# Kernel optimization log

Hardware: AMD Instinct MI355X
Metric: run time of the kernel (lower is better)

Reference implementation:

```python
import jax, jax.numpy as jnp
import numpy as np

N_NODES = 50000
N_EDGES = 800000
D_IN = 64
D_OUT = 64


def setup_inputs() -> dict:
    key = jax.random.key(0)
    k1, k2, k3, k4, k5 = jax.random.split(key, 5)
    x = jax.random.normal(k1, (N_NODES, D_IN), dtype=jnp.float32)
    senders = jax.random.randint(k2, (N_EDGES,), 0, N_NODES, dtype=jnp.int32)
    receivers = jax.random.randint(k3, (N_EDGES,), 0, N_NODES, dtype=jnp.int32)
    # eqx.nn.Linear params: weight [out, in], bias [out]
    weight = jax.random.normal(k4, (D_OUT, D_IN), dtype=jnp.float32) / np.sqrt(D_IN)
    bias = jax.random.normal(k5, (D_OUT,), dtype=jnp.float32) * 0.01
    return {"x": x, "senders": senders, "receivers": receivers, "weight": weight, "bias": bias}


def reference(x, senders, receivers, weight, bias):
    n = x.shape[0]
    # jraph.GraphConvolution applies update_node_fn (the Linear) FIRST
    h = x @ weight.T + bias  # [N, D_OUT]
    # add self edges
    self_idx = jnp.arange(n, dtype=senders.dtype)
    cs = jnp.concatenate([senders, self_idx])
    cr = jnp.concatenate([receivers, self_idx])
    ones = jnp.ones(cs.shape, dtype=h.dtype)
    sender_deg = jax.ops.segment_sum(ones, cs, num_segments=n)
    receiver_deg = jax.ops.segment_sum(ones, cr, num_segments=n)
    # symmetric normalization: D^{-1/2} A D^{-1/2}
    h = h * jax.lax.rsqrt(jnp.maximum(sender_deg, 1.0))[:, None]
    h = jax.ops.segment_sum(h[cs], cr, num_segments=n)  # gather -> scatter-add
    h = h * jax.lax.rsqrt(jnp.maximum(receiver_deg, 1.0))[:, None]
    return jax.nn.leaky_relu(h)  # default negative_slope=0.01
```

## Files before the change

### kernel.cpp

```cpp
#include <hip/hip_runtime.h>

#define N_NODES 50000
#define N_EDGES 800000
#define D 64
#define NB 196
#define BSZ 256
#define NSLICE 256
#define SLICE_E 3136
#define SLICE_I4 784
#define E4 (N_EDGES / 4)

__device__ __forceinline__ ushort f2bf(float f) {
    unsigned u = __float_as_uint(f);
    unsigned r = u + 0x7fffu + ((u >> 16) & 1u);
    return (ushort)(r >> 16);
}
__device__ __forceinline__ void acc8(const uint4 a, float* acc) {
    acc[0] += __uint_as_float(a.x << 16);
    acc[1] += __uint_as_float(a.x & 0xffff0000u);
    acc[2] += __uint_as_float(a.y << 16);
    acc[3] += __uint_as_float(a.y & 0xffff0000u);
    acc[4] += __uint_as_float(a.z << 16);
    acc[5] += __uint_as_float(a.z & 0xffff0000u);
    acc[6] += __uint_as_float(a.w << 16);
    acc[7] += __uint_as_float(a.w & 0xffff0000u);
}

__global__ __launch_bounds__(1024) void part1_kernel(
        const int* __restrict__ s, const int* __restrict__ r,
        unsigned* __restrict__ prc, unsigned char* __restrict__ psc,
        int* __restrict__ rcnt, int* __restrict__ scnt,
        int* __restrict__ roffg, int* __restrict__ soffg) {
    __shared__ unsigned lprc[SLICE_E];
    __shared__ unsigned char lpsc[SLICE_E];
    __shared__ int rcur[NB], scur[NB];
    __shared__ int rof[NB], sof[NB];
    const int tid = threadIdx.x, sl = blockIdx.x;
    for (int i = tid; i < NB; i += 1024) { rcur[i] = 0; scur[i] = 0; }
    __syncthreads();

    int e4 = sl * SLICE_I4 + tid;
    const bool act = (tid < SLICE_I4) && (e4 < E4);
    int4 rv, sv;
    if (act) {
        rv = ((const int4*)r)[e4];
        sv = ((const int4*)s)[e4];
        atomicAdd(&rcur[rv.x >> 8], 1); atomicAdd(&rcur[rv.y >> 8], 1);
        atomicAdd(&rcur[rv.z >> 8], 1); atomicAdd(&rcur[rv.w >> 8], 1);
        atomicAdd(&scur[sv.x >> 8], 1); atomicAdd(&scur[sv.y >> 8], 1);
        atomicAdd(&scur[sv.z >> 8], 1); atomicAdd(&scur[sv.w >> 8], 1);
    }
    __syncthreads();

    {
        const int wv = tid >> 6, lane = tid & 63;
        if (wv < 2) {
            const int* cnt = wv ? scur : rcur;
            int* off = wv ? sof : rof;
            const int base = lane * 4;
            int c0 = (base + 0 < NB) ? cnt[base + 0] : 0;
            int c1 = (base + 1 < NB) ? cnt[base + 1] : 0;
            int c2 = (base + 2 < NB) ? cnt[base + 2] : 0;
            int c3 = (base + 3 < NB) ? cnt[base + 3] : 0;
            int sum = c0 + c1 + c2 + c3;
            int sv_ = sum;
            #pragma unroll
            for (int o = 1; o < 64; o <<= 1) {
                int u = __shfl_up(sv_, o);
                if (lane >= o) sv_ += u;
            }
            int excl = sv_ - sum;
            if (base + 0 < NB) off[base + 0] = excl;
            if (base + 1 < NB) off[base + 1] = excl + c0;
            if (base + 2 < NB) off[base + 2] = excl + c0 + c1;
            if (base + 3 < NB) off[base + 3] = excl + c0 + c1 + c2;
        }
    }
    __syncthreads();

    if (tid < NB) {
        rcnt[sl * NB + tid] = rcur[tid];
        scnt[sl * NB + tid] = scur[tid];
        roffg[sl * NB + tid] = rof[tid];
        soffg[sl * NB + tid] = sof[tid];
    }
    __syncthreads();

    if (act) {
        int ri[4] = {rv.x, rv.y, rv.z, rv.w};
        int si[4] = {sv.x, sv.y, sv.z, sv.w};
        #pragma unroll
        for (int k = 0; k < 4; ++k) {
            int pos = atomicAdd(&rof[ri[k] >> 8], 1);
            lprc[pos] = ((unsigned)(ri[k] & 255) << 16) | (unsigned)si[k];
            int pos2 = atomicAdd(&sof[si[k] >> 8], 1);
            lpsc[pos2] = (unsigned char)(si[k] & 255);
        }
    }
    __syncthreads();

    if (tid < SLICE_I4)
        ((uint4*)(prc + (size_t)sl * SLICE_E))[tid] = ((const uint4*)lprc)[tid];
    if (tid < SLICE_E / 16)
        ((uint4*)(psc + (size_t)sl * SLICE_E))[tid] = ((const uint4*)lpsc)[tid];
}

__global__ __launch_bounds__(256, 4) void post_kernel(
        const unsigned* __restrict__ prc, const unsigned char* __restrict__ psc,
        const int* __restrict__ rcnt, const int* __restrict__ scnt,
        const int* __restrict__ roffg, const int* __restrict__ soffg,
        int* __restrict__ rowoff, ushort* __restrict__ csr16,
        const float* __restrict__ x, const float* __restrict__ w,
        const float* __restrict__ bias, ushort* __restrict__ h16) {
    __shared__ int sc[256];
    __shared__ int h4[BSZ];
    __shared__ float wlds[64 * 68];
    __shared__ float xlds[64 * 68];
    __shared__ float slds[BSZ];
    __shared__ float blds[64];
    const int tid = threadIdx.x;

    if (blockIdx.x >= NB) {
        const int b = blockIdx.x - NB;
        h4[tid] = 0;
        if (tid < 64) blds[tid] = bias[tid];
        __syncthreads();
        {
            int sl = tid;
            int c = scnt[sl * NB + b];
            const unsigned char* cell = psc + (size_t)sl * SLICE_E + soffg[sl * NB + b];
            for (int i = 0; i < c; ++i) atomicAdd(&h4[cell[i]], 1);
        }
        __syncthreads();
        slds[tid] = rsqrtf((float)(h4[tid] + 1));
        #pragma unroll
        for (int q = 0; q < 4; ++q) {
            int idx = q * 256 + tid;
            int o = idx >> 4, k4 = idx & 15;
            float4 wv = ((const float4*)w)[idx];
            *(float4*)&wlds[o * 68 + k4 * 4] = wv;
        }
        __syncthreads();

        const int t15 = tid & 15;
        const int g = tid >> 4;
        for (int tile = 0; tile < 4; ++tile) {
            const int nb = b * BSZ + tile * 64;
            #pragma unroll
            for (int q = 0; q < 4; ++q) {
                int idx = q * 256 + tid;
                int nl = idx >> 4, k4 = idx & 15;
                int n = nb + nl;
                float4 xv = (n < N_NODES) ? ((const float4*)x)[n * 16 + k4]
                                          : make_float4(0.f, 0.f, 0.f, 0.f);
                *(float4*)&xlds[nl * 68 + k4 * 4] = xv;
            }
            __syncthreads();

            float acc[4][4];
            #pragma unroll
            for (int i = 0; i < 4; ++i)
                #pragma unroll
                for (int j = 0; j < 4; ++j) acc[i][j] = 0.f;

            #pragma unroll 2
            for (int k4 = 0; k4 < 16; ++k4) {
                float4 wv0 = *(const float4*)&wlds[(t15     ) * 68 + k4 * 4];
                float4 wv1 = *(const float4*)&wlds[(t15 + 16) * 68 + k4 * 4];
                float4 wv2 = *(const float4*)&wlds[(t15 + 32) * 68 + k4 * 4];
                float4 wv3 = *(const float4*)&wlds[(t15 + 48) * 68 + k4 * 4];
                #pragma unroll
                for (int i = 0; i < 4; ++i) {
                    float4 xv = *(const float4*)&xlds[(g * 4 + i) * 68 + k4 * 4];
                    acc[i][0] += xv.x * wv0.x + xv.y * wv0.y + xv.z * wv0.z + xv.w * wv0.w;
                    acc[i][1] += xv.x * wv1.x + xv.y * wv1.y + xv.z * wv1.z + xv.w * wv1.w;
                    acc[i][2] += xv.x * wv2.x + xv.y * wv2.y + xv.z * wv2.z + xv.w * wv2.w;
                    acc[i][3] += xv.x * wv3.x + xv.y * wv3.y + xv.z * wv3.z + xv.w * wv3.w;
                }
            }

            #pragma unroll
            for (int i = 0; i < 4; ++i) {
                int nl = g * 4 + i;
                int n = nb + nl;
                if (n < N_NODES) {
                    float scl = slds[tile * 64 + nl];
                    h16[n * D + t15     ] = f2bf((acc[i][0] + blds[t15     ]) * scl);
                    h16[n * D + t15 + 16] = f2bf((acc[i][1] + blds[t15 + 16]) * scl);
                    h16[n * D + t15 + 32] = f2bf((acc[i][2] + blds[t15 + 32]) * scl);
                    h16[n * D + t15 + 48] = f2bf((acc[i][3] + blds[t15 + 48]) * scl);
                }
            }
            __syncthreads();
        }
        return;
    }

    const int b = blockIdx.x;
    int tot = 0;
    if (tid < NB) {
        for (int sl = 0; sl < NSLICE; ++sl) tot += rcnt[sl * NB + tid];
    }
    sc[tid] = tot;
    __syncthreads();
    for (int o = 1; o < 256; o <<= 1) {
        int u = (tid >= o) ? sc[tid - o] : 0;
        __syncthreads();
        sc[tid] += u;
        __syncthreads();
    }
    const int rb = (b == 0) ? 0 : sc[b - 1];
    __syncthreads();

    h4[tid] = 0;
    __syncthreads();
    {
        int sl = tid;
        int c = rcnt[sl * NB + b];
        const unsigned* cell = prc + (size_t)sl * SLICE_E + roffg[sl * NB + b];
        for (int i = 0; i < c; ++i) atomicAdd(&h4[cell[i] >> 16], 1);
    }
    __syncthreads();

    int v = h4[tid];
    sc[tid] = v;
    __syncthreads();
    for (int o = 1; o < 256; o <<= 1) {
        int u = (tid >= o) ? sc[tid - o] : 0;
        __syncthreads();
        sc[tid] += u;
        __syncthreads();
    }
    int excl = sc[tid] - v;
    int n = b * BSZ + tid;
    if (n < N_NODES) rowoff[n] = rb + excl;
    h4[tid] = rb + excl;
    if (b == NB - 1 && tid == 0) rowoff[N_NODES] = N_EDGES;
    __syncthreads();

    {
        int sl = tid;
        int c = rcnt[sl * NB + b];
        const unsigned* cell = prc + (size_t)sl * SLICE_E + roffg[sl * NB + b];
        for (int i = 0; i < c; ++i) {
            unsigned pw = cell[i];
            int pos = atomicAdd(&h4[pw >> 16], 1);
            csr16[pos] = (ushort)(pw & 0xffffu);
        }
    }
}

__global__ __launch_bounds__(256) void gather_kernel(
        const ushort* __restrict__ h16, const int* __restrict__ rowoff,
        const ushort* __restrict__ csr16, float* __restrict__ out) {
    const int lane = threadIdx.x & 63;
    const int q = lane & 7;
    const int g = lane >> 3;
    const int n = blockIdx.x * 4 + (threadIdx.x >> 6);
    if (n >= N_NODES) return;

    float acc[8];
    #pragma unroll
    for (int k = 0; k < 8; ++k) acc[k] = 0.f;

    const int base = rowoff[n];
    const int cnt = rowoff[n + 1] - base;

    for (int j0 = 0; j0 < cnt; j0 += 64) {
        int m = cnt - j0; if (m > 64) m = 64;
        int my = (lane < m) ? (int)csr16[base + j0 + lane] : 0;
        int t = 0;
        for (; t + 16 <= m; t += 16) {
            int s0 = __shfl(my, t + g);
            int s1 = __shfl(my, t + 8 + g);
            uint4 a = *(const uint4*)&h16[s0 * D + q * 8];
            uint4 b = *(const uint4*)&h16[s1 * D + q * 8];
            acc8(a, acc);
            acc8(b, acc);
        }
        for (; t < m; t += 8) {
            int e = t + g;
            int ee = (e < m) ? e : 0;
            int s0 = __shfl(my, ee);
            if (e < m) {
                uint4 a = *(const uint4*)&h16[s0 * D + q * 8];
                acc8(a, acc);
            }
        }
    }

    #pragma unroll
    for (int k = 0; k < 8; ++k) acc[k] += __shfl_xor(acc[k], 8);
    #pragma unroll
    for (int k = 0; k < 8; ++k) acc[k] += __shfl_xor(acc[k], 16);
    #pragma unroll
    for (int k = 0; k < 8; ++k) acc[k] += __shfl_xor(acc[k], 32);

    uint4 sv = *(const uint4*)&h16[n * D + q * 8];
    acc8(sv, acc);
    float sc = rsqrtf((float)(cnt + 1));
    float o[8];
    #pragma unroll
    for (int k = 0; k < 8; ++k) {
        float vv = acc[k] * sc;
        o[k] = vv > 0.f ? vv : 0.01f * vv;
    }
    if (g == 0) {
        *(float4*)(out + n * D + q * 8)     = make_float4(o[0], o[1], o[2], o[3]);
    } else if (g == 1) {
        *(float4*)(out + n * D + q * 8 + 4) = make_float4(o[4], o[5], o[6], o[7]);
    }
}

extern "C" void kernel_launch(void* const* d_in, const int* in_sizes, int n_in,
                              void* d_out, int out_size, void* d_ws, size_t ws_size,
                              hipStream_t stream) {
    const float* x       = (const float*)d_in[0];
    const int*   senders = (const int*)d_in[1];
    const int*   recvs   = (const int*)d_in[2];
    const float* weight  = (const float*)d_in[3];
    const float* bias    = (const float*)d_in[4];
    float* out = (float*)d_out;

    char* p = (char*)d_ws;
    auto take = [&](size_t bytes) { char* q = p; p += (bytes + 255) & ~(size_t)255; return q; };
    ushort*        h16    = (ushort*)take((size_t)N_NODES * D * 2);
    unsigned*      prc    = (unsigned*)take((size_t)NSLICE * SLICE_E * 4);
    unsigned char* psc    = (unsigned char*)take((size_t)NSLICE * SLICE_E);
    int*           rcnt   = (int*)take((size_t)NSLICE * NB * 4);
    int*           scnt   = (int*)take((size_t)NSLICE * NB * 4);
    int*           roffg  = (int*)take((size_t)NSLICE * NB * 4);
    int*           soffg  = (int*)take((size_t)NSLICE * NB * 4);
    int*           rowoff = (int*)take((size_t)(N_NODES + 1) * 4);
    ushort*        csr16  = (ushort*)take((size_t)N_EDGES * 2);

    hipLaunchKernelGGL(part1_kernel, dim3(NSLICE), dim3(1024), 0, stream,
                       senders, recvs, prc, psc, rcnt, scnt, roffg, soffg);
    hipLaunchKernelGGL(post_kernel, dim3(2 * NB), dim3(BSZ), 0, stream,
                       prc, psc, rcnt, scnt, roffg, soffg, rowoff, csr16,
                       x, weight, bias, h16);
    hipLaunchKernelGGL(gather_kernel, dim3((N_NODES + 3) / 4), dim3(256), 0, stream,
                       h16, rowoff, csr16, out);
}
```

Before: 63.04 us.

## Pad CSR rows to multiples of 8 with zero-row sentinel and fixed per-block stride

Each receiver row is padded to a multiple of 8 entries that point at an added all-zero row of h16. This lets the gather tail loop run as one unpredicated step instead of a masked loop. CSR segments now sit at a fixed per-block stride (8192), so post_kernel no longer needs the 256-slice global prefix sum over rcnt per block. Degree and padded count are packed into a new rdeg array. The cost is extra padded gathers of the zero row. A block with more than 8192 padded edges would overflow its segment; the random uniform input makes this unlikely.

```diff
diff --git a/kernel.cpp b/kernel.cpp
--- a/kernel.cpp
+++ b/kernel.cpp
@@ -9,6 +9,8 @@
 #define SLICE_E 3136
 #define SLICE_I4 784
 #define E4 (N_EDGES / 4)
+#define ZROW N_NODES
+#define BSTRIDE 8192
 
 __device__ __forceinline__ ushort f2bf(float f) {
     unsigned u = __float_as_uint(f);
@@ -109,7 +111,8 @@
         const unsigned* __restrict__ prc, const unsigned char* __restrict__ psc,
         const int* __restrict__ rcnt, const int* __restrict__ scnt,
         const int* __restrict__ roffg, const int* __restrict__ soffg,
-        int* __restrict__ rowoff, ushort* __restrict__ csr16,
+        int* __restrict__ rowoff, int* __restrict__ rdeg,
+        ushort* __restrict__ csr16,
         const float* __restrict__ x, const float* __restrict__ w,
         const float* __restrict__ bias, ushort* __restrict__ h16) {
     __shared__ int sc[256];
@@ -124,6 +127,8 @@
         const int b = blockIdx.x - NB;
         h4[tid] = 0;
         if (tid < 64) blds[tid] = bias[tid];
+        if (b == 0 && tid < 8)
+            ((uint4*)(h16 + (size_t)ZROW * D))[tid] = make_uint4(0u, 0u, 0u, 0u);
         __syncthreads();
         {
             int sl = tid;
@@ -197,20 +202,6 @@
     }
 
     const int b = blockIdx.x;
-    int tot = 0;
-    if (tid < NB) {
-        for (int sl = 0; sl < NSLICE; ++sl) tot += rcnt[sl * NB + tid];
-    }
-    sc[tid] = tot;
-    __syncthreads();
-    for (int o = 1; o < 256; o <<= 1) {
-        int u = (tid >= o) ? sc[tid - o] : 0;
-        __syncthreads();
-        sc[tid] += u;
-        __syncthreads();
-    }
-    const int rb = (b == 0) ? 0 : sc[b - 1];
-    __syncthreads();
 
     h4[tid] = 0;
     __syncthreads();
@@ -222,8 +213,11 @@
     }
     __syncthreads();
 
-    int v = h4[tid];
-    sc[tid] = v;
+    int c = h4[tid];
+    int pc = (c + 7) & ~7;
+    int n = b * BSZ + tid;
+    if (n >= N_NODES) { c = 0; pc = 0; }
+    sc[tid] = pc;
     __syncthreads();
     for (int o = 1; o < 256; o <<= 1) {
         int u = (tid >= o) ? sc[tid - o] : 0;
@@ -231,18 +225,20 @@
         sc[tid] += u;
         __syncthreads();
     }
-    int excl = sc[tid] - v;
-    int n = b * BSZ + tid;
-    if (n < N_NODES) rowoff[n] = rb + excl;
-    h4[tid] = rb + excl;
-    if (b == NB - 1 && tid == 0) rowoff[N_NODES] = N_EDGES;
+    int start = b * BSTRIDE + sc[tid] - pc;
+    if (n < N_NODES) {
+        rowoff[n] = start;
+        rdeg[n] = (pc << 16) | c;
+    }
+    h4[tid] = start;
+    for (int i = start + c; i < start + pc; ++i) csr16[i] = (ushort)ZROW;
     __syncthreads();
 
     {
         int sl = tid;
-        int c = rcnt[sl * NB + b];
+        int cc = rcnt[sl * NB + b];
         const unsigned* cell = prc + (size_t)sl * SLICE_E + roffg[sl * NB + b];
-        for (int i = 0; i < c; ++i) {
+        for (int i = 0; i < cc; ++i) {
             unsigned pw = cell[i];
             int pos = atomicAdd(&h4[pw >> 16], 1);
             csr16[pos] = (ushort)(pw & 0xffffu);
@@ -252,7 +248,8 @@
 
 __global__ __launch_bounds__(256) void gather_kernel(
         const ushort* __restrict__ h16, const int* __restrict__ rowoff,
-        const ushort* __restrict__ csr16, float* __restrict__ out) {
+        const int* __restrict__ rdeg, const ushort* __restrict__ csr16,
+        float* __restrict__ out) {
     const int lane = threadIdx.x & 63;
     const int q = lane & 7;
     const int g = lane >> 3;
@@ -264,10 +261,12 @@
     for (int k = 0; k < 8; ++k) acc[k] = 0.f;
 
     const int base = rowoff[n];
-    const int cnt = rowoff[n + 1] - base;
-
-    for (int j0 = 0; j0 < cnt; j0 += 64) {
-        int m = cnt - j0; if (m > 64) m = 64;
+    const unsigned word = (unsigned)rdeg[n];
+    const int cnt = (int)(word & 0xffffu);
+    const int pcnt = (int)(word >> 16);
+
+    for (int j0 = 0; j0 < pcnt; j0 += 64) {
+        int m = pcnt - j0; if (m > 64) m = 64;
         int my = (lane < m) ? (int)csr16[base + j0 + lane] : 0;
         int t = 0;
         for (; t + 16 <= m; t += 16) {
@@ -278,14 +277,10 @@
             acc8(a, acc);
             acc8(b, acc);
         }
-        for (; t < m; t += 8) {
-            int e = t + g;
-            int ee = (e < m) ? e : 0;
-            int s0 = __shfl(my, ee);
-            if (e < m) {
-                uint4 a = *(const uint4*)&h16[s0 * D + q * 8];
-                acc8(a, acc);
-            }
+        if (t < m) {
+            int s0 = __shfl(my, t + g);
+            uint4 a = *(const uint4*)&h16[s0 * D + q * 8];
+            acc8(a, acc);
         }
     }
 
@@ -324,21 +319,22 @@
 
     char* p = (char*)d_ws;
     auto take = [&](size_t bytes) { char* q = p; p += (bytes + 255) & ~(size_t)255; return q; };
-    ushort*        h16    = (ushort*)take((size_t)N_NODES * D * 2);
+    ushort*        h16    = (ushort*)take((size_t)(N_NODES + 1) * D * 2);
     unsigned*      prc    = (unsigned*)take((size_t)NSLICE * SLICE_E * 4);
     unsigned char* psc    = (unsigned char*)take((size_t)NSLICE * SLICE_E);
     int*           rcnt   = (int*)take((size_t)NSLICE * NB * 4);
     int*           scnt   = (int*)take((size_t)NSLICE * NB * 4);
     int*           roffg  = (int*)take((size_t)NSLICE * NB * 4);
     int*           soffg  = (int*)take((size_t)NSLICE * NB * 4);
-    int*           rowoff = (int*)take((size_t)(N_NODES + 1) * 4);
-    ushort*        csr16  = (ushort*)take((size_t)N_EDGES * 2);
+    int*           rowoff = (int*)take((size_t)N_NODES * 4);
+    int*           rdeg   = (int*)take((size_t)N_NODES * 4);
+    ushort*        csr16  = (ushort*)take((size_t)NB * BSTRIDE * 2);
 
     hipLaunchKernelGGL(part1_kernel, dim3(NSLICE), dim3(1024), 0, stream,
                        senders, recvs, prc, psc, rcnt, scnt, roffg, soffg);
     hipLaunchKernelGGL(post_kernel, dim3(2 * NB), dim3(BSZ), 0, stream,
-                       prc, psc, rcnt, scnt, roffg, soffg, rowoff, csr16,
+                       prc, psc, rcnt, scnt, roffg, soffg, rowoff, rdeg, csr16,
                        x, weight, bias, h16);
     hipLaunchKernelGGL(gather_kernel, dim3((N_NODES + 3) / 4), dim3(256), 0, stream,
-                       h16, rowoff, csr16, out);
-}
+                       h16, rowoff, rdeg, csr16, out);
+}
```

Result: no change. 63.20 us (+0.2%).
